# Performance work log

Measured on AMD Instinct MI355X. Metric: run time of the kernel, lower is better.

## Reference

```python
import jax, jax.numpy as jnp
import numpy as np

B, S, D_MODEL, D_QK, D_VO = 4, 2048, 1024, 128, 128
NEG = -1.0e9


def setup_inputs() -> dict:
    key = jax.random.key(0)
    k1, k2, k3, k4, k5 = jax.random.split(key, 5)
    enc = jax.random.normal(k1, (B, S, D_MODEL), dtype=jnp.float32)
    # causal mask: True means masked (masked_fill), broadcast over batch
    causal = jnp.triu(jnp.ones((S, S), dtype=bool), k=1)
    mask = jnp.broadcast_to(causal, (B, S, S))
    scale = 0.02
    W_q = jax.random.normal(k2, (D_MODEL, D_QK), dtype=jnp.float32) * scale
    W_k = jax.random.normal(k3, (D_MODEL, D_QK), dtype=jnp.float32) * scale
    W_v = jax.random.normal(k4, (D_MODEL, D_VO), dtype=jnp.float32) * scale
    W_o = jax.random.normal(k5, (D_VO, D_MODEL), dtype=jnp.float32) * scale
    return {"encodings": enc, "mask": mask, "W_q": W_q, "W_k": W_k, "W_v": W_v, "W_o": W_o}


def reference(encodings, mask, W_q, W_k, W_v, W_o):
    # q,k: [B,S,d_qk]; v: [B,S,d_vo]
    q = jnp.einsum('bsd,de->bse', encodings, W_q)
    k = jnp.einsum('bsd,de->bse', encodings, W_k)
    v = jnp.einsum('bsd,de->bse', encodings, W_v)
    sims = jnp.einsum('bqe,bke->bqk', q, k) / jnp.asarray(D_QK ** 0.5, q.dtype)
    sims = jnp.where(mask, jnp.asarray(NEG, sims.dtype), sims)
    attn = jax.nn.softmax(sims, axis=-1)  # [B,S,S]
    scores = jnp.einsum('bqk,bke->bqe', attn, v)  # [B,S,d_vo]
    return jnp.einsum('bse,ed->bsd', scores, W_o)  # [B,S,d_model]
```

## Files before the change

kernel.cpp:

```cpp
#include <hip/hip_runtime.h>
#include <hip/hip_bf16.h>
#include <stdint.h>

typedef __attribute__((ext_vector_type(8))) short short8;
typedef __attribute__((ext_vector_type(4))) float floatx4;

using bf16 = __hip_bfloat16;

#define SCALE_L2 0.12751793359133147f

__device__ inline unsigned short f2b(float f) {
    bf16 h = __float2bfloat16(f);
    return *(unsigned short*)&h;
}
__device__ inline float b2f(unsigned short u) {
    union { unsigned int i; float f; } v;
    v.i = ((unsigned int)u) << 16;
    return v.f;
}

__device__ __forceinline__ void gll16(const bf16* g, bf16* l) {
    __builtin_amdgcn_global_load_lds((__attribute__((address_space(1))) void*)g,
                                     (__attribute__((address_space(3))) void*)l,
                                     16, 0, 0);
}

__global__ __launch_bounds__(256) void prep_w(const float* __restrict__ Wq,
                                              const float* __restrict__ Wk,
                                              const float* __restrict__ Wv,
                                              const float* __restrict__ Wo,
                                              bf16* __restrict__ Wqkvt,
                                              bf16* __restrict__ Wot) {
    int idx = blockIdx.x * 256 + threadIdx.x;
    int sel = idx >> 17;
    int i = idx & 131071;
    if (sel < 3) {
        const float* W = (sel == 0) ? Wq : (sel == 1) ? Wk : Wv;
        int r = i >> 7, c = i & 127;
        Wqkvt[(size_t)(sel * 128 + c) * 1024 + r] = __float2bfloat16(W[i]);
    } else {
        int r = i >> 10, c = i & 1023;
        Wot[(size_t)c * 128 + r] = __float2bfloat16(Wo[i]);
    }
}

__global__ __launch_bounds__(256) void gemm_qkv(const float* __restrict__ enc,
                                                const bf16* __restrict__ Bt,
                                                bf16* __restrict__ Qb,
                                                bf16* __restrict__ Kb,
                                                bf16* __restrict__ Vtb) {
    __shared__ __align__(16) bf16 As[32 * 32];
    __shared__ __align__(16) bf16 Bs[128 * 32];

    const int bx = blockIdx.x;
    const int xcd = bx & 7;
    const int q = bx >> 3;
    const int t3 = q * 2731 >> 13;
    const int tile = xcd * 32 + t3;
    const int nsel = q - t3 * 3;
    const int m0 = tile * 32;
    const int brow0 = nsel * 128;

    const int tid = threadIdx.x;
    const int w = tid >> 6, lane = tid & 63;
    const int wr = (w >> 1) * 16, wc = (w & 1) * 64;
    const int quad = lane >> 4, l16 = lane & 15;

    const int ar = tid >> 3, af = tid & 7;
    const int br = w * 16 + (lane >> 2), bk = (lane & 3) * 8;

    const float4* Arow4 = (const float4*)&enc[(size_t)(m0 + ar) * 1024];
    float4 a0 = Arow4[af];

    floatx4 acc[4];
#pragma unroll
    for (int j = 0; j < 4; j++) acc[j] = (floatx4){0.f, 0.f, 0.f, 0.f};

    for (int k0 = 0; k0 < 1024; k0 += 32) {
        __syncthreads();
        gll16(&Bt[(size_t)(brow0 + br) * 1024 + k0 + bk], &Bs[w * 512]);
        gll16(&Bt[(size_t)(brow0 + 64 + br) * 1024 + k0 + bk], &Bs[2048 + w * 512]);
        ushort4 u0;
        u0.x = f2b(a0.x); u0.y = f2b(a0.y); u0.z = f2b(a0.z); u0.w = f2b(a0.w);
        *(ushort4*)&As[ar * 32 + af * 4] = u0;
        __syncthreads();

        if (k0 + 32 < 1024)
            a0 = Arow4[((k0 + 32) >> 2) + af];

        short8 a = *(const short8*)&As[(wr + l16) * 32 + quad * 8];
        short8 bfr[4];
#pragma unroll
        for (int nt = 0; nt < 4; nt++)
            bfr[nt] = *(const short8*)&Bs[(wc + nt * 16 + l16) * 32 + quad * 8];
#pragma unroll
        for (int nt = 0; nt < 4; nt++)
            acc[nt] = __builtin_amdgcn_mfma_f32_16x16x32_bf16(a, bfr[nt], acc[nt], 0, 0, 0);
    }

    if (nsel < 2) {
        bf16* D = (nsel == 0) ? Qb : Kb;
#pragma unroll
        for (int nt = 0; nt < 4; nt++)
#pragma unroll
            for (int r = 0; r < 4; r++) {
                int row = m0 + wr + quad * 4 + r;
                int col = wc + nt * 16 + l16;
                D[(size_t)row * 128 + col] = __float2bfloat16(acc[nt][r]);
            }
    } else {
        const int row0 = m0 + wr + quad * 4;
        const int bb = row0 >> 11, ss = row0 & 2047;
#pragma unroll
        for (int nt = 0; nt < 4; nt++) {
            int col = wc + nt * 16 + l16;
            ushort4 pk;
            pk.x = f2b(acc[nt][0]); pk.y = f2b(acc[nt][1]);
            pk.z = f2b(acc[nt][2]); pk.w = f2b(acc[nt][3]);
            *(ushort4*)&Vtb[(size_t)bb * 262144 + (size_t)col * 2048 + ss] = pk;
        }
    }
}

__global__ __launch_bounds__(256) void gemm_out(const bf16* __restrict__ A,
                                                const bf16* __restrict__ Bt,
                                                float* __restrict__ C) {
    __shared__ bf16 As[64 * 40];
    __shared__ bf16 Bs[128 * 40];

    const int tid = threadIdx.x;
    const int m0 = blockIdx.x * 64;
    const int n0 = blockIdx.y * 128;
    const int w = tid >> 6, lane = tid & 63;
    const int wm = (w >> 1) * 32, wn = (w & 1) * 64;
    const int quad = lane >> 4, l16 = lane & 15;

    const int ra = tid >> 2, ca = (tid & 3) * 8;
    const int rb0 = tid >> 2, rb1 = (tid + 256) >> 2;

    floatx4 acc[2][4];
#pragma unroll
    for (int i = 0; i < 2; i++)
#pragma unroll
        for (int j = 0; j < 4; j++) acc[i][j] = (floatx4){0.f, 0.f, 0.f, 0.f};

    int4 pa  = *(const int4*)&A[(size_t)(m0 + ra) * 128 + ca];
    int4 pb0 = *(const int4*)&Bt[(size_t)(n0 + rb0) * 128 + ca];
    int4 pb1 = *(const int4*)&Bt[(size_t)(n0 + rb1) * 128 + ca];

    for (int k0 = 0; k0 < 128; k0 += 32) {
        __syncthreads();
        *(int4*)&As[ra * 40 + ca] = pa;
        *(int4*)&Bs[rb0 * 40 + ca] = pb0;
        *(int4*)&Bs[rb1 * 40 + ca] = pb1;
        __syncthreads();

        if (k0 + 32 < 128) {
            pa  = *(const int4*)&A[(size_t)(m0 + ra) * 128 + k0 + 32 + ca];
            pb0 = *(const int4*)&Bt[(size_t)(n0 + rb0) * 128 + k0 + 32 + ca];
            pb1 = *(const int4*)&Bt[(size_t)(n0 + rb1) * 128 + k0 + 32 + ca];
        }

        short8 a[2], b[4];
#pragma unroll
        for (int mt = 0; mt < 2; mt++)
            a[mt] = *(const short8*)&As[(wm + mt * 16 + l16) * 40 + quad * 8];
#pragma unroll
        for (int nt = 0; nt < 4; nt++)
            b[nt] = *(const short8*)&Bs[(wn + nt * 16 + l16) * 40 + quad * 8];
#pragma unroll
        for (int mt = 0; mt < 2; mt++)
#pragma unroll
            for (int nt = 0; nt < 4; nt++)
                acc[mt][nt] = __builtin_amdgcn_mfma_f32_16x16x32_bf16(a[mt], b[nt], acc[mt][nt], 0, 0, 0);
    }

#pragma unroll
    for (int mt = 0; mt < 2; mt++)
#pragma unroll
        for (int nt = 0; nt < 4; nt++)
#pragma unroll
            for (int r = 0; r < 4; r++) {
                int row = m0 + wm + mt * 16 + quad * 4 + r;
                int col = n0 + wn + nt * 16 + l16;
                C[(size_t)row * 1024 + col] = acc[mt][nt][r];
            }
}

__global__ __launch_bounds__(512) void flash_split(const bf16* __restrict__ Q,
                                                   const bf16* __restrict__ K,
                                                   const bf16* __restrict__ Vt,
                                                   bf16* __restrict__ Opb,
                                                   float2* __restrict__ Ml) {
    __shared__ __align__(16) char smem[51200];

    const int tid = threadIdx.x;
    const int x = blockIdx.x;
    const int b = x / 136;
    const int id = x - b * 136;
    int qt = (int)((__builtin_amdgcn_sqrtf(8.0f * (float)id + 1.0f) - 1.0f) * 0.5f);
    if (qt < 0) qt = 0;
    while ((qt + 1) * (qt + 2) / 2 <= id) qt++;
    while (qt * (qt + 1) / 2 > id) qt--;
    const int c = id - qt * (qt + 1) / 2;
    const int q0 = qt * 128;
    const int start = 2 * c;
    const int end = min(start + 2, 2 * qt + 2);

    const int w = tid >> 6, lane = tid & 63;
    const int quad = lane >> 4, l16 = lane & 15;
    bf16* Ks = (bf16*)smem;
    bf16* Vs = (bf16*)(smem + 16384);
    bf16* myP = (bf16*)(smem + 32768) + w * 1152;

    const int krow = w * 4 + (lane >> 4);
    const int kcb  = (lane & 15) * 16;
    const int vrow = w * 8 + (lane >> 3);
    const int vcb  = (lane & 7) * 16;
    const int ksw  = (l16 & 7) << 4;

    const int qrow = q0 + w * 16 + l16;
    const bf16* Qrow = &Q[((size_t)b * 2048 + qrow) * 128];
    short8 qf[4];
#pragma unroll
    for (int k4 = 0; k4 < 4; k4++)
        qf[k4] = *(const short8*)&Qrow[k4 * 32 + quad * 8];

    float m_run = -1.0e30f, l_run = 0.f;
    floatx4 o[8];
#pragma unroll
    for (int d = 0; d < 8; d++) o[d] = (floatx4){0.f, 0.f, 0.f, 0.f};

    {
        const int kt = start;
#pragma unroll
        for (int i = 0; i < 2; i++) {
            int row = i * 32 + krow;
            int cbs = kcb ^ ((row & 7) << 4);
            gll16(&K[((size_t)b * 2048 + kt * 64 + row) * 128 + (cbs >> 1)],
                  &Ks[i * 4096 + w * 512]);
        }
#pragma unroll
        for (int i = 0; i < 2; i++) {
            int row = i * 64 + vrow;
            int cbs = vcb ^ ((row & 7) << 4);
            gll16(&Vt[(size_t)b * 262144 + (size_t)row * 2048 + kt * 64 + (cbs >> 1)],
                  &Vs[i * 4096 + w * 512]);
        }
    }
    __syncthreads();

    for (int kt = start; kt < end; kt++) {
        floatx4 s_acc[4];
#pragma unroll
        for (int nt = 0; nt < 4; nt++) {
            s_acc[nt] = (floatx4){0.f, 0.f, 0.f, 0.f};
#pragma unroll
            for (int k4 = 0; k4 < 4; k4++) {
                short8 kf = *(const short8*)((const char*)Ks +
                              (nt * 16 + l16) * 256 + ((k4 * 64 + quad * 16) ^ ksw));
                s_acc[nt] = __builtin_amdgcn_mfma_f32_16x16x32_bf16(kf, qf[k4], s_acc[nt], 0, 0, 0);
            }
        }

        float sv[4][4];
        const bool diag = (kt >= 2 * qt);
#pragma unroll
        for (int nt = 0; nt < 4; nt++)
#pragma unroll
            for (int r = 0; r < 4; r++) {
                float s = s_acc[nt][r] * SCALE_L2;
                if (diag) {
                    int kcol = kt * 64 + nt * 16 + quad * 4 + r;
                    if (kcol > qrow) s = -1.0e9f;
                }
                sv[nt][r] = s;
            }

        float t0 = fmaxf(fmaxf(sv[0][0], sv[0][1]), fmaxf(sv[0][2], sv[0][3]));
        float t1 = fmaxf(fmaxf(sv[1][0], sv[1][1]), fmaxf(sv[1][2], sv[1][3]));
        float t2 = fmaxf(fmaxf(sv[2][0], sv[2][1]), fmaxf(sv[2][2], sv[2][3]));
        float t3 = fmaxf(fmaxf(sv[3][0], sv[3][1]), fmaxf(sv[3][2], sv[3][3]));
        float tmax = fmaxf(fmaxf(t0, t1), fmaxf(t2, t3));
        tmax = fmaxf(tmax, __shfl_xor(tmax, 16));
        tmax = fmaxf(tmax, __shfl_xor(tmax, 32));

        float mnew = fmaxf(m_run, tmax);
        float alpha = exp2f(m_run - mnew);
        m_run = mnew;

        float rsum = 0.f;
#pragma unroll
        for (int nt = 0; nt < 4; nt++)
#pragma unroll
            for (int r = 0; r < 4; r++) {
                float p = exp2f(sv[nt][r] - mnew);
                sv[nt][r] = p;
                rsum += p;
            }
        rsum += __shfl_xor(rsum, 16);
        rsum += __shfl_xor(rsum, 32);
        l_run = l_run * alpha + rsum;

#pragma unroll
        for (int nt = 0; nt < 4; nt++) {
            ushort4 pk;
            pk.x = f2b(sv[nt][0]); pk.y = f2b(sv[nt][1]);
            pk.z = f2b(sv[nt][2]); pk.w = f2b(sv[nt][3]);
            *(ushort4*)&myP[l16 * 72 + nt * 16 + quad * 4] = pk;
        }

#pragma unroll
        for (int d = 0; d < 8; d++) {
            o[d][0] *= alpha; o[d][1] *= alpha; o[d][2] *= alpha; o[d][3] *= alpha;
        }

        short8 pf[2];
#pragma unroll
        for (int k2 = 0; k2 < 2; k2++)
            pf[k2] = *(const short8*)&myP[l16 * 72 + k2 * 32 + quad * 8];
#pragma unroll
        for (int d = 0; d < 8; d++)
#pragma unroll
            for (int k2 = 0; k2 < 2; k2++) {
                short8 vf = *(const short8*)((const char*)Vs +
                              (d * 16 + l16) * 128 + ((k2 * 64 + quad * 16) ^ ksw));
                o[d] = __builtin_amdgcn_mfma_f32_16x16x32_bf16(vf, pf[k2], o[d], 0, 0, 0);
            }

        if (kt + 1 < end) {
            __syncthreads();
            const int nk = kt + 1;
#pragma unroll
            for (int i = 0; i < 2; i++) {
                int row = i * 32 + krow;
                int cbs = kcb ^ ((row & 7) << 4);
                gll16(&K[((size_t)b * 2048 + nk * 64 + row) * 128 + (cbs >> 1)],
                      &Ks[i * 4096 + w * 512]);
            }
#pragma unroll
            for (int i = 0; i < 2; i++) {
                int row = i * 64 + vrow;
                int cbs = vcb ^ ((row & 7) << 4);
                gll16(&Vt[(size_t)b * 262144 + (size_t)row * 2048 + nk * 64 + (cbs >> 1)],
                      &Vs[i * 4096 + w * 512]);
            }
            __syncthreads();
        }
    }

    __syncthreads();
    bf16* myO = (bf16*)(smem + w * 4352);
#pragma unroll
    for (int d = 0; d < 8; d++) {
        ushort4 pk;
        pk.x = f2b(o[d][0]); pk.y = f2b(o[d][1]);
        pk.z = f2b(o[d][2]); pk.w = f2b(o[d][3]);
        *(ushort4*)&myO[l16 * 136 + d * 16 + quad * 4] = pk;
    }
    const int er = lane >> 2;
    const int ec = lane & 3;
    const size_t orow = ((size_t)x * 128 + w * 16 + er) * 128;
#pragma unroll
    for (int p = 0; p < 4; p++) {
        int ce = (p * 4 + ec) * 8;
        short8 t = *(const short8*)&myO[er * 136 + ce];
        *(short8*)&Opb[orow + ce] = t;
    }
    if (lane < 16) Ml[(size_t)x * 128 + w * 16 + l16] = make_float2(m_run, l_run);
}

__global__ __launch_bounds__(256) void flash_merge(const bf16* __restrict__ Opb,
                                                   const float2* __restrict__ Ml,
                                                   bf16* __restrict__ Sc) {
    int idx = blockIdx.x * 256 + threadIdx.x;
    int row = idx >> 5, dg = (idx & 31) * 4;
    int b = row >> 11, s = row & 2047;
    int qt = s >> 7, rl = s & 127;
    int nc = qt + 1;
    int id0 = b * 136 + qt * (qt + 1) / 2;

    float M = -1.0e30f;
    for (int j = 0; j < nc; j++)
        M = fmaxf(M, Ml[(size_t)(id0 + j) * 128 + rl].x);

    float L = 0.f;
    float a0 = 0.f, a1 = 0.f, a2 = 0.f, a3 = 0.f;
    for (int j = 0; j < nc; j++) {
        float2 t = Ml[(size_t)(id0 + j) * 128 + rl];
        float wj = exp2f(t.x - M);
        L += t.y * wj;
        ushort4 p = *(const ushort4*)&Opb[((size_t)(id0 + j) * 128 + rl) * 128 + dg];
        a0 += wj * b2f(p.x); a1 += wj * b2f(p.y);
        a2 += wj * b2f(p.z); a3 += wj * b2f(p.w);
    }
    float inv = 1.0f / L;
    ushort4 o;
    o.x = f2b(a0 * inv); o.y = f2b(a1 * inv);
    o.z = f2b(a2 * inv); o.w = f2b(a3 * inv);
    *(ushort4*)&Sc[(size_t)row * 128 + dg] = o;
}

extern "C" void kernel_launch(void* const* d_in, const int* in_sizes, int n_in,
                              void* d_out, int out_size, void* d_ws, size_t ws_size,
                              hipStream_t stream) {
    const float* enc = (const float*)d_in[0];
    const float* Wq = (const float*)d_in[2];
    const float* Wk = (const float*)d_in[3];
    const float* Wv = (const float*)d_in[4];
    const float* Wo = (const float*)d_in[5];
    float* out = (float*)d_out;

    const size_t MB = 1024 * 1024;
    char* ws = (char*)d_ws;
    bf16*   Qb    = (bf16*)(ws);
    bf16*   Kb    = (bf16*)(ws + 2 * MB);
    bf16*   Vtb   = (bf16*)(ws + 4 * MB);
    bf16*   Scb   = (bf16*)(ws + 6 * MB);
    bf16*   Wqkvt = (bf16*)(ws + 8 * MB);
    bf16*   Wot   = (bf16*)(ws + 8 * MB + 768 * 1024);
    float2* Ml    = (float2*)(ws + 9 * MB);
    bf16*   Opb   = (bf16*)(ws + 10 * MB);

    prep_w<<<2048, dim3(256), 0, stream>>>(Wq, Wk, Wv, Wo, Wqkvt, Wot);

    gemm_qkv<<<768, dim3(256), 0, stream>>>(enc, Wqkvt, Qb, Kb, Vtb);

    flash_split<<<544, dim3(512), 0, stream>>>(Qb, Kb, Vtb, Opb, Ml);
    flash_merge<<<1024, dim3(256), 0, stream>>>(Opb, Ml, Scb);

    gemm_out<<<dim3(128, 8), dim3(256), 0, stream>>>(Scb, Wot, out);
}
```

Baseline: 189.5 us.

## Fuse flash-attention partial merge into output projection GEMM

Replaces the separate merge kernel and output GEMM with one kernel. Each block merges the split partial outputs for 64 rows into shared memory, then loops over all 8 output column tiles. This removes the intermediate bf16 scores buffer round trip and one launch. In exchange the grid shrinks from 1024 to 128 blocks, which leaves many CUs idle. The weight-tile global loads also lose the register prefetch the old GEMM had.

```diff
diff --git a/kernel.cpp b/kernel.cpp
--- a/kernel.cpp
+++ b/kernel.cpp
@@ -122,71 +122,6 @@
     }
 }
 
-__global__ __launch_bounds__(256) void gemm_out(const bf16* __restrict__ A,
-                                                const bf16* __restrict__ Bt,
-                                                float* __restrict__ C) {
-    __shared__ bf16 As[64 * 40];
-    __shared__ bf16 Bs[128 * 40];
-
-    const int tid = threadIdx.x;
-    const int m0 = blockIdx.x * 64;
-    const int n0 = blockIdx.y * 128;
-    const int w = tid >> 6, lane = tid & 63;
-    const int wm = (w >> 1) * 32, wn = (w & 1) * 64;
-    const int quad = lane >> 4, l16 = lane & 15;
-
-    const int ra = tid >> 2, ca = (tid & 3) * 8;
-    const int rb0 = tid >> 2, rb1 = (tid + 256) >> 2;
-
-    floatx4 acc[2][4];
-#pragma unroll
-    for (int i = 0; i < 2; i++)
-#pragma unroll
-        for (int j = 0; j < 4; j++) acc[i][j] = (floatx4){0.f, 0.f, 0.f, 0.f};
-
-    int4 pa  = *(const int4*)&A[(size_t)(m0 + ra) * 128 + ca];
-    int4 pb0 = *(const int4*)&Bt[(size_t)(n0 + rb0) * 128 + ca];
-    int4 pb1 = *(const int4*)&Bt[(size_t)(n0 + rb1) * 128 + ca];
-
-    for (int k0 = 0; k0 < 128; k0 += 32) {
-        __syncthreads();
-        *(int4*)&As[ra * 40 + ca] = pa;
-        *(int4*)&Bs[rb0 * 40 + ca] = pb0;
-        *(int4*)&Bs[rb1 * 40 + ca] = pb1;
-        __syncthreads();
-
-        if (k0 + 32 < 128) {
-            pa  = *(const int4*)&A[(size_t)(m0 + ra) * 128 + k0 + 32 + ca];
-            pb0 = *(const int4*)&Bt[(size_t)(n0 + rb0) * 128 + k0 + 32 + ca];
-            pb1 = *(const int4*)&Bt[(size_t)(n0 + rb1) * 128 + k0 + 32 + ca];
-        }
-
-        short8 a[2], b[4];
-#pragma unroll
-        for (int mt = 0; mt < 2; mt++)
-            a[mt] = *(const short8*)&As[(wm + mt * 16 + l16) * 40 + quad * 8];
-#pragma unroll
-        for (int nt = 0; nt < 4; nt++)
-            b[nt] = *(const short8*)&Bs[(wn + nt * 16 + l16) * 40 + quad * 8];
-#pragma unroll
-        for (int mt = 0; mt < 2; mt++)
-#pragma unroll
-            for (int nt = 0; nt < 4; nt++)
-                acc[mt][nt] = __builtin_amdgcn_mfma_f32_16x16x32_bf16(a[mt], b[nt], acc[mt][nt], 0, 0, 0);
-    }
-
-#pragma unroll
-    for (int mt = 0; mt < 2; mt++)
-#pragma unroll
-        for (int nt = 0; nt < 4; nt++)
-#pragma unroll
-            for (int r = 0; r < 4; r++) {
-                int row = m0 + wm + mt * 16 + quad * 4 + r;
-                int col = n0 + wn + nt * 16 + l16;
-                C[(size_t)row * 1024 + col] = acc[mt][nt][r];
-            }
-}
-
 __global__ __launch_bounds__(512) void flash_split(const bf16* __restrict__ Q,
                                                    const bf16* __restrict__ K,
                                                    const bf16* __restrict__ Vt,
@@ -370,35 +305,105 @@
     if (lane < 16) Ml[(size_t)x * 128 + w * 16 + l16] = make_float2(m_run, l_run);
 }
 
-__global__ __launch_bounds__(256) void flash_merge(const bf16* __restrict__ Opb,
-                                                   const float2* __restrict__ Ml,
-                                                   bf16* __restrict__ Sc) {
-    int idx = blockIdx.x * 256 + threadIdx.x;
-    int row = idx >> 5, dg = (idx & 31) * 4;
-    int b = row >> 11, s = row & 2047;
-    int qt = s >> 7, rl = s & 127;
-    int nc = qt + 1;
-    int id0 = b * 136 + qt * (qt + 1) / 2;
-
-    float M = -1.0e30f;
-    for (int j = 0; j < nc; j++)
-        M = fmaxf(M, Ml[(size_t)(id0 + j) * 128 + rl].x);
-
-    float L = 0.f;
-    float a0 = 0.f, a1 = 0.f, a2 = 0.f, a3 = 0.f;
-    for (int j = 0; j < nc; j++) {
-        float2 t = Ml[(size_t)(id0 + j) * 128 + rl];
-        float wj = exp2f(t.x - M);
-        L += t.y * wj;
-        ushort4 p = *(const ushort4*)&Opb[((size_t)(id0 + j) * 128 + rl) * 128 + dg];
-        a0 += wj * b2f(p.x); a1 += wj * b2f(p.y);
-        a2 += wj * b2f(p.z); a3 += wj * b2f(p.w);
-    }
-    float inv = 1.0f / L;
-    ushort4 o;
-    o.x = f2b(a0 * inv); o.y = f2b(a1 * inv);
-    o.z = f2b(a2 * inv); o.w = f2b(a3 * inv);
-    *(ushort4*)&Sc[(size_t)row * 128 + dg] = o;
+__global__ __launch_bounds__(256) void gemm_out_fused(const bf16* __restrict__ Opb,
+                                                      const float2* __restrict__ Ml,
+                                                      const bf16* __restrict__ Bt,
+                                                      float* __restrict__ C) {
+    __shared__ __align__(16) bf16 As[64 * 132];
+    __shared__ __align__(16) bf16 Bs[128 * 40];
+
+    const int tid = threadIdx.x;
+    const int m0 = blockIdx.x * 64;
+    const int b = m0 >> 11;
+    const int s0 = m0 & 2047;
+    const int qt = s0 >> 7;
+    const int nc = qt + 1;
+    const int id0 = b * 136 + qt * (qt + 1) / 2;
+    const int rl0 = s0 & 127;
+
+    {
+        const int r = tid >> 2, g = tid & 3;
+        const int rl = rl0 + r;
+        float M = -1.0e30f;
+        for (int j = 0; j < nc; j++)
+            M = fmaxf(M, Ml[(size_t)(id0 + j) * 128 + rl].x);
+
+        float a[32];
+#pragma unroll
+        for (int i = 0; i < 32; i++) a[i] = 0.f;
+        float L = 0.f;
+        for (int j = 0; j < nc; j++) {
+            float2 t = Ml[(size_t)(id0 + j) * 128 + rl];
+            float wj = exp2f(t.x - M);
+            L += t.y * wj;
+            const bf16* src = &Opb[((size_t)(id0 + j) * 128 + rl) * 128 + g * 32];
+#pragma unroll
+            for (int u = 0; u < 4; u++) {
+                short8 p = *(const short8*)&src[u * 8];
+#pragma unroll
+                for (int e = 0; e < 8; e++)
+                    a[u * 8 + e] += wj * b2f((unsigned short)p[e]);
+            }
+        }
+        float inv = 1.0f / L;
+        bf16* dst = &As[r * 132 + g * 32];
+#pragma unroll
+        for (int u = 0; u < 4; u++) {
+            short8 pk;
+#pragma unroll
+            for (int e = 0; e < 8; e++)
+                pk[e] = (short)f2b(a[u * 8 + e] * inv);
+            *(short8*)&dst[u * 8] = pk;
+        }
+    }
+
+    const int w = tid >> 6, lane = tid & 63;
+    const int wm = (w >> 1) * 32, wn = (w & 1) * 64;
+    const int quad = lane >> 4, l16 = lane & 15;
+    const int rb0 = tid >> 2, cb = (tid & 3) * 8;
+    const int rb1 = (tid + 256) >> 2;
+
+    __syncthreads();
+
+    for (int ot = 0; ot < 8; ot++) {
+        const int n0 = ot * 128;
+        floatx4 acc[2][4];
+#pragma unroll
+        for (int i = 0; i < 2; i++)
+#pragma unroll
+            for (int j = 0; j < 4; j++) acc[i][j] = (floatx4){0.f, 0.f, 0.f, 0.f};
+
+        for (int k0 = 0; k0 < 128; k0 += 32) {
+            __syncthreads();
+            *(int4*)&Bs[rb0 * 40 + cb] = *(const int4*)&Bt[(size_t)(n0 + rb0) * 128 + k0 + cb];
+            *(int4*)&Bs[rb1 * 40 + cb] = *(const int4*)&Bt[(size_t)(n0 + rb1) * 128 + k0 + cb];
+            __syncthreads();
+
+            short8 a[2], bfr[4];
+#pragma unroll
+            for (int mt = 0; mt < 2; mt++)
+                a[mt] = *(const short8*)&As[(wm + mt * 16 + l16) * 132 + k0 + quad * 8];
+#pragma unroll
+            for (int nt = 0; nt < 4; nt++)
+                bfr[nt] = *(const short8*)&Bs[(wn + nt * 16 + l16) * 40 + quad * 8];
+#pragma unroll
+            for (int mt = 0; mt < 2; mt++)
+#pragma unroll
+                for (int nt = 0; nt < 4; nt++)
+                    acc[mt][nt] = __builtin_amdgcn_mfma_f32_16x16x32_bf16(a[mt], bfr[nt], acc[mt][nt], 0, 0, 0);
+        }
+
+#pragma unroll
+        for (int mt = 0; mt < 2; mt++)
+#pragma unroll
+            for (int nt = 0; nt < 4; nt++)
+#pragma unroll
+                for (int r = 0; r < 4; r++) {
+                    int row = m0 + wm + mt * 16 + quad * 4 + r;
+                    int col = n0 + wn + nt * 16 + l16;
+                    C[(size_t)row * 1024 + col] = acc[mt][nt][r];
+                }
+    }
 }
 
 extern "C" void kernel_launch(void* const* d_in, const int* in_sizes, int n_in,
@@ -416,7 +421,6 @@
     bf16*   Qb    = (bf16*)(ws);
     bf16*   Kb    = (bf16*)(ws + 2 * MB);
     bf16*   Vtb   = (bf16*)(ws + 4 * MB);
-    bf16*   Scb   = (bf16*)(ws + 6 * MB);
     bf16*   Wqkvt = (bf16*)(ws + 8 * MB);
     bf16*   Wot   = (bf16*)(ws + 8 * MB + 768 * 1024);
     float2* Ml    = (float2*)(ws + 9 * MB);
@@ -427,7 +431,6 @@
     gemm_qkv<<<768, dim3(256), 0, stream>>>(enc, Wqkvt, Qb, Kb, Vtb);
 
     flash_split<<<544, dim3(512), 0, stream>>>(Qb, Kb, Vtb, Opb, Ml);
-    flash_merge<<<1024, dim3(256), 0, stream>>>(Opb, Ml, Scb);
-
-    gemm_out<<<dim3(128, 8), dim3(256), 0, stream>>>(Scb, Wot, out);
-}
+
+    gemm_out_fused<<<128, dim3(256), 0, stream>>>(Opb, Ml, Wot, out);
+}
```

Result: slower. 195.2 us (+3.0%).
